# Performance work log

Hardware: AMD Instinct MI355X
Metric: run time of the kernel (lower is better)

## Reference

```python
import jax, jax.numpy as jnp
import numpy as np

N_NODES = 50000
N_EDGES = 1_600_000
HIDDEN = 128
BOND = 16


def setup_inputs() -> dict:
    key = jax.random.key(0)
    ks = jax.random.split(key, 6)
    h = jax.random.normal(ks[0], (N_NODES, HIDDEN), dtype=jnp.float32)
    edge_index = jax.random.randint(ks[1], (2, N_EDGES), 0, N_NODES, dtype=jnp.int32)
    bond_features = jax.random.normal(ks[2], (N_EDGES, BOND), dtype=jnp.float32)
    fan_in1 = 2 * HIDDEN + BOND
    W1 = jax.random.normal(ks[3], (fan_in1, HIDDEN), dtype=jnp.float32) / np.sqrt(fan_in1)
    b1 = jnp.zeros((HIDDEN,), dtype=jnp.float32)
    W2 = jax.random.normal(ks[4], (HIDDEN, HIDDEN), dtype=jnp.float32) / np.sqrt(HIDDEN)
    b2 = jnp.zeros((HIDDEN,), dtype=jnp.float32)
    return {"h": h, "edge_index": edge_index, "bond_features": bond_features,
            "W1": W1, "b1": b1, "W2": W2, "b2": b2}


def reference(h, edge_index, bond_features, W1, b1, W2, b2):
    row, col = edge_index[0], edge_index[1]
    # gather endpoint features + bond features -> [E, 2H+B]
    msgs = jnp.concatenate([h[row], h[col], bond_features], axis=-1)
    # 2-layer MLP with SiLU
    msgs = jax.nn.silu(msgs @ W1 + b1) @ W2 + b2  # [E, H]
    # scatter-add back to source nodes (index_add_ on row)
    h_out = jax.ops.segment_sum(msgs, row, num_segments=h.shape[0])
    return h_out
```

## Files before the change

### kernel.cpp

```cpp
#include <hip/hip_runtime.h>

typedef __attribute__((ext_vector_type(4))) float  f32x4;
typedef __attribute__((ext_vector_type(2))) float  f32x2;
typedef __attribute__((ext_vector_type(8))) short  s16x8;
typedef __attribute__((ext_vector_type(4))) float  f4v;
typedef __attribute__((ext_vector_type(4))) int    i32x4;

#define MFMA_BF16 __builtin_amdgcn_mfma_f32_16x16x32_bf16
#define SENT 0x7fffffff

#if defined(__has_builtin)
#if __has_builtin(__builtin_amdgcn_cvt_pk_fp8_f32) && __has_builtin(__builtin_amdgcn_cvt_pk_f32_fp8)
#define HW8 1
#endif
#endif

__device__ __forceinline__ short f2bf(float f) {
  unsigned u = __builtin_bit_cast(unsigned, f);
  u += 0x7fffu + ((u >> 16) & 1u);
  return (short)(u >> 16);
}
__device__ __forceinline__ float bf2f(short s) {
  unsigned u = ((unsigned)(unsigned short)s) << 16;
  return __builtin_bit_cast(float, u);
}
__device__ __forceinline__ s16x8 cvt8(f4v f0, f4v f1) {
  s16x8 r;
  r[0] = f2bf(f0[0]); r[1] = f2bf(f0[1]); r[2] = f2bf(f0[2]); r[3] = f2bf(f0[3]);
  r[4] = f2bf(f1[0]); r[5] = f2bf(f1[1]); r[6] = f2bf(f1[2]); r[7] = f2bf(f1[3]);
  return r;
}
__device__ __forceinline__ unsigned cvtpk_bf16(float a, float b) {
  unsigned r;
  asm("v_cvt_pk_bf16_f32 %0, %1, %2" : "=v"(r) : "v"(a), "v"(b));
  return r;
}
__device__ __forceinline__ unsigned f2fp8(float x) {
  unsigned u = __builtin_bit_cast(unsigned, x);
  unsigned s = (u >> 24) & 0x80u;
  unsigned au = u & 0x7fffffffu;
  if (au < 0x3C800000u) return s;
  unsigned biased = au - 0x3C000000u;
  unsigned val = biased >> 20;
  unsigned rem = biased & 0xFFFFFu;
  val += (rem > 0x80000u) || (rem == 0x80000u && (val & 1u));
  if (val > 0x7Eu) val = 0x7Eu;
  return s | val;
}
__device__ __forceinline__ float fp8tof(unsigned b) {
  unsigned em = b & 0x7fu;
  unsigned f = ((em + 960u) << 20) | ((b & 0x80u) << 24);
  return (em < 8u) ? 0.f : __builtin_bit_cast(float, f);
}
__device__ __forceinline__ unsigned char enc_fp8(float x) {
#ifdef HW8
  return (unsigned char)(__builtin_amdgcn_cvt_pk_fp8_f32(x, x, 0u, false) & 0xffu);
#else
  return (unsigned char)f2fp8(x);
#endif
}
__device__ __forceinline__ void dec_fp8x4(unsigned d, float* f) {
#ifdef HW8
  f32x2 lo = __builtin_amdgcn_cvt_pk_f32_fp8(d, false);
  f32x2 hi = __builtin_amdgcn_cvt_pk_f32_fp8(d, true);
  f[0] = lo[0]; f[1] = lo[1]; f[2] = hi[0]; f[3] = hi[1];
#else
#pragma unroll
  for (int j = 0; j < 4; ++j) f[j] = fp8tof((d >> (8 * j)) & 0xffu);
#endif
}

__global__ __launch_bounds__(256) void prep_weights(
    const float* __restrict__ W1, const float* __restrict__ W2,
    short* __restrict__ wp) {
  int t = blockIdx.x * 256 + threadIdx.x;
  int chunk = t >> 6, l = t & 63;
  if (chunk >= 104) return;
  int q = l >> 4, c = l & 15;
  s16x8 v;
  if (chunk < 72) {
    int kk = chunk >> 3, nt = chunk & 7;
    int k0 = kk * 32 + q * 8, n = nt * 16 + c;
#pragma unroll
    for (int j = 0; j < 8; ++j) {
      int k = k0 + j;
      v[j] = (k < 272) ? f2bf(W1[k * 128 + n]) : (short)0;
    }
    *reinterpret_cast<s16x8*>(wp + (size_t)chunk * 512 + l * 8) = v;
  } else {
    int c2 = chunk - 72;
    int kk = c2 >> 3, nt = c2 & 7;
    int k0 = kk * 32 + q * 8, n = nt * 16 + c;
#pragma unroll
    for (int j = 0; j < 8; ++j) v[j] = f2bf(W2[(k0 + j) * 128 + n]);
    *reinterpret_cast<s16x8*>(wp + 36864 + (size_t)c2 * 512 + l * 8) = v;
  }
}

#define NB_H 512
__global__ __launch_bounds__(256) void k_gh(
    const float* __restrict__ h, const short* __restrict__ wp,
    short* __restrict__ Gs, const int* __restrict__ ei,
    int* __restrict__ cnt, int NN, int NB_G, int E) {
  if ((int)blockIdx.x >= NB_G) {
    int i = ((int)blockIdx.x - NB_G) * 256 + threadIdx.x;
    for (; i < E; i += NB_H * 256) atomicAdd(&cnt[ei[i]], 1);
    return;
  }
  const int tid = threadIdx.x;
  const int w = tid >> 6, l = tid & 63;
  const int q = l >> 4, c = l & 15;
  const int nb = blockIdx.x * 64 + w * 16;

  f32x4 acc[16];
#pragma unroll
  for (int nt = 0; nt < 16; ++nt) acc[nt] = (f32x4){0.f, 0.f, 0.f, 0.f};

#pragma unroll
  for (int kk = 0; kk < 4; ++kk) {
    int node = nb + c; if (node >= NN) node = NN - 1;
    const float* src = h + (size_t)node * 128 + kk * 32 + q * 8;
    s16x8 a = cvt8(*reinterpret_cast<const f4v*>(src),
                   *reinterpret_cast<const f4v*>(src + 4));
#pragma unroll
    for (int nt2 = 0; nt2 < 16; ++nt2) {
      int kkg = kk + ((nt2 >= 8) ? 4 : 0);
      int chunk = kkg * 8 + (nt2 & 7);
      s16x8 b = *reinterpret_cast<const s16x8*>(wp + (size_t)chunk * 512 + l * 8);
      acc[nt2] = MFMA_BF16(a, b, acc[nt2], 0, 0, 0);
    }
  }
  unsigned char* Gb = (unsigned char*)Gs;
#pragma unroll
  for (int nt2 = 0; nt2 < 16; ++nt2)
#pragma unroll
    for (int r = 0; r < 4; ++r) {
      int node = nb + q * 4 + r;
      if (node < NN) {
        if (nt2 < 8) {
          Gs[(size_t)node * 192 + nt2 * 16 + c] = f2bf(acc[nt2][r]);
        } else {
          int n7 = nt2 - 8;
          int addr = ((n7 & 1) * 2 + (c >> 3)) * 32 + (n7 >> 1) * 8 + (c & 7);
          Gb[(size_t)node * 384 + 256 + addr] = enc_fp8(acc[nt2][r]);
        }
      }
    }
}

__global__ __launch_bounds__(1024) void k_s1(const int* __restrict__ cnt,
                                             int* __restrict__ partial, int NN) {
  __shared__ int red[16];
  int t = threadIdx.x, idx = blockIdx.x * 1024 + t;
  int v = (idx < NN) ? cnt[idx] : 0;
#pragma unroll
  for (int d = 1; d < 64; d <<= 1) v += __shfl_xor(v, d);
  if ((t & 63) == 0) red[t >> 6] = v;
  __syncthreads();
  if (t == 0) {
    int s = 0;
#pragma unroll
    for (int i = 0; i < 16; ++i) s += red[i];
    partial[blockIdx.x] = s;
  }
}
__global__ __launch_bounds__(1024) void k_s2(int* __restrict__ partial, int P) {
  __shared__ int ps[1024];
  int t = threadIdx.x;
  int v = (t < P) ? partial[t] : 0;
  ps[t] = v; __syncthreads();
  for (int d = 1; d < 1024; d <<= 1) {
    int u = (t >= d) ? ps[t - d] : 0;
    __syncthreads(); ps[t] += u; __syncthreads();
  }
  if (t < P) partial[t] = ps[t] - v;
}
__global__ __launch_bounds__(1024) void k_s3(int* __restrict__ cnt,
                                             const int* __restrict__ partial, int NN) {
  __shared__ int ps[1024];
  int t = threadIdx.x, idx = blockIdx.x * 1024 + t;
  int v = (idx < NN) ? cnt[idx] : 0;
  ps[t] = v; __syncthreads();
  for (int d = 1; d < 1024; d <<= 1) {
    int u = (t >= d) ? ps[t - d] : 0;
    __syncthreads(); ps[t] += u; __syncthreads();
  }
  if (idx < NN) cnt[idx] = ps[t] - v + partial[blockIdx.x];
}

__global__ void k_scatter8(const int* __restrict__ ei, int* __restrict__ cnt,
                           int* __restrict__ rc, short* __restrict__ bond_s,
                           const float* __restrict__ bond, int E) {
  int i = blockIdx.x * blockDim.x + threadIdx.x;
  int stride = gridDim.x * blockDim.x;
  for (; i < E; i += stride) {
    int r = ei[i], c = ei[(size_t)E + i];
    int pos = atomicAdd(&cnt[r], 1);
    rc[pos] = r | (c << 16);
    const f4v* b4 = reinterpret_cast<const f4v*>(bond + (size_t)i * 16);
    s16x8 lo = cvt8(b4[0], b4[1]);
    s16x8 hi = cvt8(b4[2], b4[3]);
    s16x8* dst = reinterpret_cast<s16x8*>(bond_s + (size_t)pos * 16);
    dst[0] = lo;
    dst[1] = hi;
  }
}

__global__ void k_scatter(const int* __restrict__ ei, int* __restrict__ cnt,
                          int2* __restrict__ rce, int E) {
  int i = blockIdx.x * blockDim.x + threadIdx.x;
  int stride = gridDim.x * blockDim.x;
  for (; i < E; i += stride) {
    int r = ei[i], c = ei[(size_t)E + i];
    int pos = atomicAdd(&cnt[r], 1);
    rce[pos] = make_int2(r | (c << 16), i);
  }
}

__global__ __launch_bounds__(256, 4) void edge_mlp8(
    const short* __restrict__ Gs, const int* __restrict__ rc,
    const short* __restrict__ bond_s, const short* __restrict__ wp,
    const float* __restrict__ b1, const float* __restrict__ b2,
    float* __restrict__ out, int E) {
  __shared__ __align__(16) char ubuf[4 * 16 * 136 * 2];
  short (*Plds)[16][136] = reinterpret_cast<short(*)[16][136]>(ubuf);
  float (*Sred)[16][68]  = reinterpret_cast<float(*)[16][68]>(ubuf);
  __shared__ int rows_s[64];
  __shared__ int cols_s[64];

  const int tid = threadIdx.x;
  const int w = tid >> 6, l = tid & 63;
  const int q = l >> 4, c = l & 15;

  int nwg = gridDim.x;
  int qq = nwg >> 3, rr = nwg & 7;
  int xcd = blockIdx.x & 7, idx = blockIdx.x >> 3;
  int sbid = (xcd < rr ? xcd * (qq + 1) : rr * (qq + 1) + (xcd - rr) * qq) + idx;
  const int eb = sbid * 64;

  if (tid < 64) {
    int gpos = eb + tid;
    if (gpos < E) {
      int v = rc[gpos];
      rows_s[tid] = v & 0xffff;
      cols_s[tid] = ((unsigned)v) >> 16;
    } else {
      rows_s[tid] = SENT; cols_s[tid] = 0;
    }
  }
  __syncthreads();

  const int we = w * 16;
  int el = we + c;
  int rv = rows_s[el];
  int rA = (rv == SENT) ? 0 : rv;
  int cA = cols_s[el];

  unsigned long long bm = __ballot(
      (l < 16) && (rows_s[we + l] != ((l < 15) ? rows_s[we + l + 1] : -1)));

  s16x8 g1v[4];
  i32x4 g2v[2];
  s16x8 az = {};
  {
    const short* gb = Gs + (size_t)rA * 192;
#pragma unroll
    for (int kk = 0; kk < 4; ++kk)
      g1v[kk] = *reinterpret_cast<const s16x8*>(gb + kk * 32 + q * 8);
    const char* g2b = (const char*)Gs + (size_t)cA * 384 + 256 + q * 32;
    g2v[0] = *reinterpret_cast<const i32x4*>(g2b);
    g2v[1] = *reinterpret_cast<const i32x4*>(g2b + 16);
    if (q < 2) {
      int ge = eb + we + c; if (ge >= E) ge = E - 1;
      az = *reinterpret_cast<const s16x8*>(bond_s + (size_t)ge * 16 + q * 8);
    }
  }

  f32x4 accb[8];
#pragma unroll
  for (int nt = 0; nt < 8; ++nt) accb[nt] = (f32x4){0.f, 0.f, 0.f, 0.f};
#pragma unroll
  for (int nt = 0; nt < 8; ++nt) {
    s16x8 b = *reinterpret_cast<const s16x8*>(wp + (size_t)(64 + nt) * 512 + l * 8);
    accb[nt] = MFMA_BF16(az, b, accb[nt], 0, 0, 0);
  }

#pragma unroll
  for (int nt = 0; nt < 8; ++nt) {
    float bias = b1[nt * 16 + c];
#pragma unroll
    for (int r = 0; r < 4; ++r)
      Plds[w][q * 4 + r][nt * 16 + c] = f2bf(accb[nt][r] + bias);
  }

  f32x4 acc2[8];
#pragma unroll
  for (int nt = 0; nt < 8; ++nt) acc2[nt] = (f32x4){0.f, 0.f, 0.f, 0.f};

#pragma unroll
  for (int kk = 0; kk < 4; ++kk) {
    s16x8 gk = g1v[kk];
    unsigned d0 = (unsigned)g2v[kk >> 1][(kk & 1) * 2 + 0];
    unsigned d1 = (unsigned)g2v[kk >> 1][(kk & 1) * 2 + 1];
    float g2f[8];
    dec_fp8x4(d0, g2f);
    dec_fp8x4(d1, g2f + 4);
    s16x8 pb = *reinterpret_cast<const s16x8*>(&Plds[w][c][kk * 32 + q * 8]);
    float sv[8];
#pragma unroll
    for (int j = 0; j < 8; ++j) {
      float x = bf2f(gk[j]) + g2f[j] + bf2f(pb[j]);
      float e = __expf(-x);
      sv[j] = x * __builtin_amdgcn_rcpf(1.f + e);
    }
    i32x4 a2w;
#pragma unroll
    for (int p = 0; p < 4; ++p)
      a2w[p] = (int)cvtpk_bf16(sv[2 * p], sv[2 * p + 1]);
    s16x8 a2 = __builtin_bit_cast(s16x8, a2w);
#pragma unroll
    for (int nt = 0; nt < 8; ++nt) {
      s16x8 b = *reinterpret_cast<const s16x8*>(wp + 36864 + (size_t)(kk * 8 + nt) * 512 + l * 8);
      acc2[nt] = MFMA_BF16(a2, b, acc2[nt], 0, 0, 0);
    }
  }

#pragma unroll
  for (int h2 = 0; h2 < 2; ++h2) {
    if (h2) __syncthreads();
#pragma unroll
    for (int nt2 = 0; nt2 < 4; ++nt2) {
      int nt = h2 * 4 + nt2;
      float bias = b2[nt * 16 + c];
#pragma unroll
      for (int r = 0; r < 4; ++r)
        Sred[w][q * 4 + r][nt2 * 16 + c] = acc2[nt][r] + bias;
    }
    float vsum = 0.f;
#pragma unroll
    for (int r = 0; r < 16; ++r) {
      vsum += Sred[w][r][l];
      if ((bm >> r) & 1ull) {
        int rowv = rows_s[we + r];
        if (rowv != SENT)
          unsafeAtomicAdd(&out[(size_t)rowv * 128 + h2 * 64 + l], vsum);
        vsum = 0.f;
      }
    }
  }
}

__global__ __launch_bounds__(256, 4) void edge_mlp7(
    const short* __restrict__ Gs, const int2* __restrict__ rce,
    const float* __restrict__ bond, const short* __restrict__ wp,
    const float* __restrict__ b1, const float* __restrict__ b2,
    float* __restrict__ out, int E) {
  __shared__ __align__(16) char ubuf[4 * 16 * 136 * 2];
  short (*Plds)[16][136] = reinterpret_cast<short(*)[16][136]>(ubuf);
  float (*Sred)[16][68]  = reinterpret_cast<float(*)[16][68]>(ubuf);
  __shared__ int rows_s[64];
  __shared__ int cols_s[64];
  __shared__ int eidx_s[64];

  const int tid = threadIdx.x;
  const int w = tid >> 6, l = tid & 63;
  const int q = l >> 4, c = l & 15;

  int nwg = gridDim.x;
  int qq = nwg >> 3, rr = nwg & 7;
  int xcd = blockIdx.x & 7, idx = blockIdx.x >> 3;
  int sbid = (xcd < rr ? xcd * (qq + 1) : rr * (qq + 1) + (xcd - rr) * qq) + idx;
  const int eb = sbid * 64;

  if (tid < 64) {
    int gpos = eb + tid;
    if (gpos < E) {
      int2 v = rce[gpos];
      rows_s[tid] = v.x & 0xffff;
      cols_s[tid] = ((unsigned)v.x) >> 16;
      eidx_s[tid] = v.y;
    } else {
      rows_s[tid] = SENT; cols_s[tid] = 0; eidx_s[tid] = 0;
    }
  }
  __syncthreads();

  const int we = w * 16;
  int el = we + c;
  int rv = rows_s[el];
  int rA = (rv == SENT) ? 0 : rv;
  int cA = cols_s[el];
  int eA = eidx_s[el];

  unsigned long long bm = __ballot(
      (l < 16) && (rows_s[we + l] != ((l < 15) ? rows_s[we + l + 1] : -1)));

  s16x8 g1v[4];
  i32x4 g2v[2];
  {
    const short* gb = Gs + (size_t)rA * 192;
#pragma unroll
    for (int kk = 0; kk < 4; ++kk)
      g1v[kk] = *reinterpret_cast<const s16x8*>(gb + kk * 32 + q * 8);
    const char* g2b = (const char*)Gs + (size_t)cA * 384 + 256 + q * 32;
    g2v[0] = *reinterpret_cast<const i32x4*>(g2b);
    g2v[1] = *reinterpret_cast<const i32x4*>(g2b + 16);
  }

  f32x4 accb[8];
#pragma unroll
  for (int nt = 0; nt < 8; ++nt) accb[nt] = (f32x4){0.f, 0.f, 0.f, 0.f};
  {
    s16x8 a = {};
    if (q < 2) {
      const float* src = bond + (size_t)eA * 16 + q * 8;
      a = cvt8(*reinterpret_cast<const f4v*>(src),
               *reinterpret_cast<const f4v*>(src + 4));
    }
#pragma unroll
    for (int nt = 0; nt < 8; ++nt) {
      s16x8 b = *reinterpret_cast<const s16x8*>(wp + (size_t)(64 + nt) * 512 + l * 8);
      accb[nt] = MFMA_BF16(a, b, accb[nt], 0, 0, 0);
    }
  }

#pragma unroll
  for (int nt = 0; nt < 8; ++nt) {
    float bias = b1[nt * 16 + c];
#pragma unroll
    for (int r = 0; r < 4; ++r)
      Plds[w][q * 4 + r][nt * 16 + c] = f2bf(accb[nt][r] + bias);
  }

  f32x4 acc2[8];
#pragma unroll
  for (int nt = 0; nt < 8; ++nt) acc2[nt] = (f32x4){0.f, 0.f, 0.f, 0.f};

#pragma unroll
  for (int kk = 0; kk < 4; ++kk) {
    s16x8 gk = g1v[kk];
    unsigned d0 = (unsigned)g2v[kk >> 1][(kk & 1) * 2 + 0];
    unsigned d1 = (unsigned)g2v[kk >> 1][(kk & 1) * 2 + 1];
    float g2f[8];
    dec_fp8x4(d0, g2f);
    dec_fp8x4(d1, g2f + 4);
    s16x8 pb = *reinterpret_cast<const s16x8*>(&Plds[w][c][kk * 32 + q * 8]);
    s16x8 a2;
#pragma unroll
    for (int j = 0; j < 8; ++j) {
      float x = bf2f(gk[j]) + g2f[j] + bf2f(pb[j]);
      float e = __expf(-x);
      float s = x * __builtin_amdgcn_rcpf(1.f + e);
      a2[j] = f2bf(s);
    }
#pragma unroll
    for (int nt = 0; nt < 8; ++nt) {
      s16x8 b = *reinterpret_cast<const s16x8*>(wp + 36864 + (size_t)(kk * 8 + nt) * 512 + l * 8);
      acc2[nt] = MFMA_BF16(a2, b, acc2[nt], 0, 0, 0);
    }
  }

#pragma unroll
  for (int h2 = 0; h2 < 2; ++h2) {
    if (h2) __syncthreads();
#pragma unroll
    for (int nt2 = 0; nt2 < 4; ++nt2) {
      int nt = h2 * 4 + nt2;
      float bias = b2[nt * 16 + c];
#pragma unroll
      for (int r = 0; r < 4; ++r)
        Sred[w][q * 4 + r][nt2 * 16 + c] = acc2[nt][r] + bias;
    }
    float vsum = 0.f;
#pragma unroll
    for (int r = 0; r < 16; ++r) {
      vsum += Sred[w][r][l];
      if ((bm >> r) & 1ull) {
        int rowv = rows_s[we + r];
        if (rowv != SENT)
          unsafeAtomicAdd(&out[(size_t)rowv * 128 + h2 * 64 + l], vsum);
        vsum = 0.f;
      }
    }
  }
}

__global__ __launch_bounds__(256, 2) void edge_mlp(
    const float* __restrict__ h, const int* __restrict__ ei,
    const float* __restrict__ bond, const short* __restrict__ wp,
    const float* __restrict__ b1, const float* __restrict__ b2,
    float* __restrict__ out, int E) {
  __shared__ __align__(16) short Plds[4][64][136];
  __shared__ int rows_s[256];
  __shared__ int cols_s[256];
  const int tid = threadIdx.x;
  const int w = tid >> 6, l = tid & 63;
  const int q = l >> 4, c = l & 15;
  const int eb = blockIdx.x * 256;
  {
    int e = eb + tid; if (e >= E) e = E - 1;
    rows_s[tid] = ei[e];
    cols_s[tid] = ei[(size_t)E + e];
  }
  __syncthreads();
  const int we = w * 64;
  int rN[4], cN[4], eI[4];
#pragma unroll
  for (int mi = 0; mi < 4; ++mi) {
    int el = we + mi * 16 + c;
    rN[mi] = rows_s[el]; cN[mi] = cols_s[el];
    int eg = eb + el; if (eg >= E) eg = E - 1;
    eI[mi] = eg;
  }
  f32x4 acc[4][8];
#pragma unroll
  for (int mi = 0; mi < 4; ++mi)
#pragma unroll
    for (int nt = 0; nt < 8; ++nt) acc[mi][nt] = (f32x4){0.f, 0.f, 0.f, 0.f};
#pragma unroll
  for (int part = 0; part < 2; ++part) {
#pragma unroll
    for (int kk = 0; kk < 4; ++kk) {
      s16x8 a[4];
#pragma unroll
      for (int mi = 0; mi < 4; ++mi) {
        int node = part ? cN[mi] : rN[mi];
        const float* src = h + (size_t)node * 128 + kk * 32 + q * 8;
        a[mi] = cvt8(*reinterpret_cast<const f4v*>(src),
                     *reinterpret_cast<const f4v*>(src + 4));
      }
      const int kkg = part * 4 + kk;
#pragma unroll
      for (int nt = 0; nt < 8; ++nt) {
        s16x8 b = *reinterpret_cast<const s16x8*>(wp + (size_t)(kkg * 8 + nt) * 512 + l * 8);
#pragma unroll
        for (int mi = 0; mi < 4; ++mi)
          acc[mi][nt] = MFMA_BF16(a[mi], b, acc[mi][nt], 0, 0, 0);
      }
    }
  }
  {
    s16x8 a[4];
#pragma unroll
    for (int mi = 0; mi < 4; ++mi) {
      s16x8 az = {};
      if (q < 2) {
        const float* src = bond + (size_t)eI[mi] * 16 + q * 8;
        az = cvt8(*reinterpret_cast<const f4v*>(src),
                  *reinterpret_cast<const f4v*>(src + 4));
      }
      a[mi] = az;
    }
#pragma unroll
    for (int nt = 0; nt < 8; ++nt) {
      s16x8 b = *reinterpret_cast<const s16x8*>(wp + (size_t)(64 + nt) * 512 + l * 8);
#pragma unroll
      for (int mi = 0; mi < 4; ++mi)
        acc[mi][nt] = MFMA_BF16(a[mi], b, acc[mi][nt], 0, 0, 0);
    }
  }
#pragma unroll
  for (int nt = 0; nt < 8; ++nt) {
    float bias = b1[nt * 16 + c];
#pragma unroll
    for (int mi = 0; mi < 4; ++mi)
#pragma unroll
      for (int r = 0; r < 4; ++r) {
        float x = acc[mi][nt][r] + bias;
        float s = x / (1.f + __expf(-x));
        Plds[w][mi * 16 + q * 4 + r][nt * 16 + c] = f2bf(s);
      }
  }
  f32x4 acc2[4][8];
#pragma unroll
  for (int mi = 0; mi < 4; ++mi)
#pragma unroll
    for (int nt = 0; nt < 8; ++nt) acc2[mi][nt] = (f32x4){0.f, 0.f, 0.f, 0.f};
#pragma unroll
  for (int kk = 0; kk < 4; ++kk) {
    s16x8 a2[4];
#pragma unroll
    for (int mi = 0; mi < 4; ++mi)
      a2[mi] = *reinterpret_cast<const s16x8*>(&Plds[w][mi * 16 + c][kk * 32 + q * 8]);
#pragma unroll
    for (int nt = 0; nt < 8; ++nt) {
      s16x8 b = *reinterpret_cast<const s16x8*>(wp + 36864 + (size_t)(kk * 8 + nt) * 512 + l * 8);
#pragma unroll
      for (int mi = 0; mi < 4; ++mi)
        acc2[mi][nt] = MFMA_BF16(a2[mi], b, acc2[mi][nt], 0, 0, 0);
    }
  }
#pragma unroll
  for (int nt = 0; nt < 8; ++nt) {
    float bias = b2[nt * 16 + c];
#pragma unroll
    for (int mi = 0; mi < 4; ++mi)
#pragma unroll
      for (int r = 0; r < 4; ++r) {
        int el = we + mi * 16 + q * 4 + r;
        if ((eb + el) < E) {
          int node = rows_s[el];
          unsafeAtomicAdd(&out[(size_t)node * 128 + nt * 16 + c],
                          acc2[mi][nt][r] + bias);
        }
      }
  }
}

extern "C" void kernel_launch(void* const* d_in, const int* in_sizes, int n_in,
                              void* d_out, int out_size, void* d_ws, size_t ws_size,
                              hipStream_t stream) {
  const float* h    = (const float*)d_in[0];
  const int*   ei   = (const int*)d_in[1];
  const float* bond = (const float*)d_in[2];
  const float* W1   = (const float*)d_in[3];
  const float* b1   = (const float*)d_in[4];
  const float* W2   = (const float*)d_in[5];
  const float* b2   = (const float*)d_in[6];
  float* out = (float*)d_out;
  char* ws = (char*)d_ws;

  const int E  = in_sizes[1] / 2;
  const int NN = in_sizes[0] / 128;

  short* wp = (short*)ws;
  size_t off_G    = 131072;
  size_t off_cnt  = off_G + (size_t)NN * 384;
  size_t off_par  = off_cnt + (((size_t)NN * 4 + 15) & ~15ull);
  size_t off_idx  = off_par + 4096;
  size_t off_bs   = off_idx + (((size_t)E * 4 + 15) & ~15ull);
  size_t need8    = off_bs + (size_t)E * 32;
  size_t need7    = off_idx + (size_t)E * 8;

  hipMemsetAsync(d_out, 0, (size_t)NN * 128 * sizeof(float), stream);
  prep_weights<<<26, 256, 0, stream>>>(W1, W2, wp);

  if (ws_size >= need8 && NN <= 65535) {
    short* Gs     = (short*)(ws + off_G);
    int*   cnt    = (int*)(ws + off_cnt);
    int*   par    = (int*)(ws + off_par);
    int*   rc     = (int*)(ws + off_idx);
    short* bond_s = (short*)(ws + off_bs);
    const int NB_G = (NN + 63) / 64;
    const int P    = (NN + 1023) / 1024;

    hipMemsetAsync(cnt, 0, (size_t)NN * 4, stream);
    k_gh<<<NB_G + NB_H, 256, 0, stream>>>(h, wp, Gs, ei, cnt, NN, NB_G, E);
    k_s1<<<P, 1024, 0, stream>>>(cnt, par, NN);
    k_s2<<<1, 1024, 0, stream>>>(par, P);
    k_s3<<<P, 1024, 0, stream>>>(cnt, par, NN);
    k_scatter8<<<2048, 256, 0, stream>>>(ei, cnt, rc, bond_s, bond, E);
    edge_mlp8<<<(E + 63) / 64, 256, 0, stream>>>(Gs, rc, bond_s, wp, b1, b2, out, E);
  } else if (ws_size >= need7 && NN <= 65535) {
    short* Gs   = (short*)(ws + off_G);
    int*   cnt  = (int*)(ws + off_cnt);
    int*   par  = (int*)(ws + off_par);
    int2*  rce  = (int2*)(ws + off_idx);
    const int NB_G = (NN + 63) / 64;
    const int P    = (NN + 1023) / 1024;

    hipMemsetAsync(cnt, 0, (size_t)NN * 4, stream);
    k_gh<<<NB_G + NB_H, 256, 0, stream>>>(h, wp, Gs, ei, cnt, NN, NB_G, E);
    k_s1<<<P, 1024, 0, stream>>>(cnt, par, NN);
    k_s2<<<1, 1024, 0, stream>>>(par, P);
    k_s3<<<P, 1024, 0, stream>>>(cnt, par, NN);
    k_scatter<<<2048, 256, 0, stream>>>(ei, cnt, rce, E);
    edge_mlp7<<<(E + 63) / 64, 256, 0, stream>>>(Gs, rce, bond, wp, b1, b2, out, E);
  } else {
    edge_mlp<<<(E + 255) / 256, 256, 0, stream>>>(h, ei, bond, wp, b1, b2, out, E);
  }
}
```

Before: 440.3 us.

## Process two 64-edge groups per block with all gathers issued upfront

Each block of the edge MLP kernel now handles 128 sorted edges instead of 64. The node-feature, fp8 column-feature and bond gathers for both groups are issued before any compute, so the second group's memory latency is hidden behind the first group's MFMA work, and weight reloads are spread over twice as many edges. The cost is higher register pressure from holding two sets of gathered operands, which could cause spills or lower occupancy under the 256x4 launch bounds, and the grid has half as many blocks.

```diff
diff --git a/kernel.cpp b/kernel.cpp
--- a/kernel.cpp
+++ b/kernel.cpp
@@ -217,7 +217,7 @@
   }
 }
 
-__global__ __launch_bounds__(256, 4) void edge_mlp8(
+__global__ __launch_bounds__(256, 4) void edge_mlp9(
     const short* __restrict__ Gs, const int* __restrict__ rc,
     const short* __restrict__ bond_s, const short* __restrict__ wp,
     const float* __restrict__ b1, const float* __restrict__ b2,
@@ -225,8 +225,8 @@
   __shared__ __align__(16) char ubuf[4 * 16 * 136 * 2];
   short (*Plds)[16][136] = reinterpret_cast<short(*)[16][136]>(ubuf);
   float (*Sred)[16][68]  = reinterpret_cast<float(*)[16][68]>(ubuf);
-  __shared__ int rows_s[64];
-  __shared__ int cols_s[64];
+  __shared__ int rows_s[128];
+  __shared__ int cols_s[128];
 
   const int tid = threadIdx.x;
   const int w = tid >> 6, l = tid & 63;
@@ -236,9 +236,9 @@
   int qq = nwg >> 3, rr = nwg & 7;
   int xcd = blockIdx.x & 7, idx = blockIdx.x >> 3;
   int sbid = (xcd < rr ? xcd * (qq + 1) : rr * (qq + 1) + (xcd - rr) * qq) + idx;
-  const int eb = sbid * 64;
-
-  if (tid < 64) {
+  const int eb = sbid * 128;
+
+  if (tid < 128) {
     int gpos = eb + tid;
     if (gpos < E) {
       int v = rc[gpos];
@@ -251,100 +251,113 @@
   __syncthreads();
 
   const int we = w * 16;
-  int el = we + c;
-  int rv = rows_s[el];
-  int rA = (rv == SENT) ? 0 : rv;
-  int cA = cols_s[el];
-
-  unsigned long long bm = __ballot(
-      (l < 16) && (rows_s[we + l] != ((l < 15) ? rows_s[we + l + 1] : -1)));
-
-  s16x8 g1v[4];
-  i32x4 g2v[2];
-  s16x8 az = {};
-  {
-    const short* gb = Gs + (size_t)rA * 192;
+  int rA[2], cA[2];
+  unsigned long long bm[2];
+#pragma unroll
+  for (int g = 0; g < 2; ++g) {
+    int el = g * 64 + we + c;
+    int rv = rows_s[el];
+    rA[g] = (rv == SENT) ? 0 : rv;
+    cA[g] = cols_s[el];
+    bm[g] = __ballot(
+        (l < 16) &&
+        (rows_s[g * 64 + we + l] != ((l < 15) ? rows_s[g * 64 + we + l + 1] : -1)));
+  }
+
+  s16x8 g1v[2][4];
+  i32x4 g2v[2][2];
+  s16x8 az[2];
+#pragma unroll
+  for (int g = 0; g < 2; ++g) {
+    const short* gb = Gs + (size_t)rA[g] * 192;
 #pragma unroll
     for (int kk = 0; kk < 4; ++kk)
-      g1v[kk] = *reinterpret_cast<const s16x8*>(gb + kk * 32 + q * 8);
-    const char* g2b = (const char*)Gs + (size_t)cA * 384 + 256 + q * 32;
-    g2v[0] = *reinterpret_cast<const i32x4*>(g2b);
-    g2v[1] = *reinterpret_cast<const i32x4*>(g2b + 16);
+      g1v[g][kk] = *reinterpret_cast<const s16x8*>(gb + kk * 32 + q * 8);
+    const char* g2b = (const char*)Gs + (size_t)cA[g] * 384 + 256 + q * 32;
+    g2v[g][0] = *reinterpret_cast<const i32x4*>(g2b);
+    g2v[g][1] = *reinterpret_cast<const i32x4*>(g2b + 16);
+    s16x8 a0 = {};
     if (q < 2) {
-      int ge = eb + we + c; if (ge >= E) ge = E - 1;
-      az = *reinterpret_cast<const s16x8*>(bond_s + (size_t)ge * 16 + q * 8);
-    }
-  }
-
-  f32x4 accb[8];
-#pragma unroll
-  for (int nt = 0; nt < 8; ++nt) accb[nt] = (f32x4){0.f, 0.f, 0.f, 0.f};
-#pragma unroll
-  for (int nt = 0; nt < 8; ++nt) {
-    s16x8 b = *reinterpret_cast<const s16x8*>(wp + (size_t)(64 + nt) * 512 + l * 8);
-    accb[nt] = MFMA_BF16(az, b, accb[nt], 0, 0, 0);
-  }
-
-#pragma unroll
-  for (int nt = 0; nt < 8; ++nt) {
-    float bias = b1[nt * 16 + c];
-#pragma unroll
-    for (int r = 0; r < 4; ++r)
-      Plds[w][q * 4 + r][nt * 16 + c] = f2bf(accb[nt][r] + bias);
-  }
-
-  f32x4 acc2[8];
-#pragma unroll
-  for (int nt = 0; nt < 8; ++nt) acc2[nt] = (f32x4){0.f, 0.f, 0.f, 0.f};
-
-#pragma unroll
-  for (int kk = 0; kk < 4; ++kk) {
-    s16x8 gk = g1v[kk];
-    unsigned d0 = (unsigned)g2v[kk >> 1][(kk & 1) * 2 + 0];
-    unsigned d1 = (unsigned)g2v[kk >> 1][(kk & 1) * 2 + 1];
-    float g2f[8];
-    dec_fp8x4(d0, g2f);
-    dec_fp8x4(d1, g2f + 4);
-    s16x8 pb = *reinterpret_cast<const s16x8*>(&Plds[w][c][kk * 32 + q * 8]);
-    float sv[8];
-#pragma unroll
-    for (int j = 0; j < 8; ++j) {
-      float x = bf2f(gk[j]) + g2f[j] + bf2f(pb[j]);
-      float e = __expf(-x);
-      sv[j] = x * __builtin_amdgcn_rcpf(1.f + e);
-    }
-    i32x4 a2w;
-#pragma unroll
-    for (int p = 0; p < 4; ++p)
-      a2w[p] = (int)cvtpk_bf16(sv[2 * p], sv[2 * p + 1]);
-    s16x8 a2 = __builtin_bit_cast(s16x8, a2w);
+      int ge = eb + g * 64 + we + c; if (ge >= E) ge = E - 1;
+      a0 = *reinterpret_cast<const s16x8*>(bond_s + (size_t)ge * 16 + q * 8);
+    }
+    az[g] = a0;
+  }
+
+#pragma unroll
+  for (int g = 0; g < 2; ++g) {
+    if (g) __syncthreads();
+
+    f32x4 accb[8];
+#pragma unroll
+    for (int nt = 0; nt < 8; ++nt) accb[nt] = (f32x4){0.f, 0.f, 0.f, 0.f};
 #pragma unroll
     for (int nt = 0; nt < 8; ++nt) {
-      s16x8 b = *reinterpret_cast<const s16x8*>(wp + 36864 + (size_t)(kk * 8 + nt) * 512 + l * 8);
-      acc2[nt] = MFMA_BF16(a2, b, acc2[nt], 0, 0, 0);
-    }
-  }
-
-#pragma unroll
-  for (int h2 = 0; h2 < 2; ++h2) {
-    if (h2) __syncthreads();
-#pragma unroll
-    for (int nt2 = 0; nt2 < 4; ++nt2) {
-      int nt = h2 * 4 + nt2;
-      float bias = b2[nt * 16 + c];
+      s16x8 b = *reinterpret_cast<const s16x8*>(wp + (size_t)(64 + nt) * 512 + l * 8);
+      accb[nt] = MFMA_BF16(az[g], b, accb[nt], 0, 0, 0);
+    }
+
+#pragma unroll
+    for (int nt = 0; nt < 8; ++nt) {
+      float bias = b1[nt * 16 + c];
 #pragma unroll
       for (int r = 0; r < 4; ++r)
-        Sred[w][q * 4 + r][nt2 * 16 + c] = acc2[nt][r] + bias;
-    }
-    float vsum = 0.f;
-#pragma unroll
-    for (int r = 0; r < 16; ++r) {
-      vsum += Sred[w][r][l];
-      if ((bm >> r) & 1ull) {
-        int rowv = rows_s[we + r];
-        if (rowv != SENT)
-          unsafeAtomicAdd(&out[(size_t)rowv * 128 + h2 * 64 + l], vsum);
-        vsum = 0.f;
+        Plds[w][q * 4 + r][nt * 16 + c] = f2bf(accb[nt][r] + bias);
+    }
+
+    f32x4 acc2[8];
+#pragma unroll
+    for (int nt = 0; nt < 8; ++nt) acc2[nt] = (f32x4){0.f, 0.f, 0.f, 0.f};
+
+#pragma unroll
+    for (int kk = 0; kk < 4; ++kk) {
+      s16x8 gk = g1v[g][kk];
+      unsigned d0 = (unsigned)g2v[g][kk >> 1][(kk & 1) * 2 + 0];
+      unsigned d1 = (unsigned)g2v[g][kk >> 1][(kk & 1) * 2 + 1];
+      float g2f[8];
+      dec_fp8x4(d0, g2f);
+      dec_fp8x4(d1, g2f + 4);
+      s16x8 pb = *reinterpret_cast<const s16x8*>(&Plds[w][c][kk * 32 + q * 8]);
+      float sv[8];
+#pragma unroll
+      for (int j = 0; j < 8; ++j) {
+        float x = bf2f(gk[j]) + g2f[j] + bf2f(pb[j]);
+        float e = __expf(-x);
+        sv[j] = x * __builtin_amdgcn_rcpf(1.f + e);
+      }
+      i32x4 a2w;
+#pragma unroll
+      for (int p = 0; p < 4; ++p)
+        a2w[p] = (int)cvtpk_bf16(sv[2 * p], sv[2 * p + 1]);
+      s16x8 a2 = __builtin_bit_cast(s16x8, a2w);
+#pragma unroll
+      for (int nt = 0; nt < 8; ++nt) {
+        s16x8 b = *reinterpret_cast<const s16x8*>(wp + 36864 + (size_t)(kk * 8 + nt) * 512 + l * 8);
+        acc2[nt] = MFMA_BF16(a2, b, acc2[nt], 0, 0, 0);
+      }
+    }
+
+#pragma unroll
+    for (int h2 = 0; h2 < 2; ++h2) {
+      if (h2) __syncthreads();
+#pragma unroll
+      for (int nt2 = 0; nt2 < 4; ++nt2) {
+        int nt = h2 * 4 + nt2;
+        float bias = b2[nt * 16 + c];
+#pragma unroll
+        for (int r = 0; r < 4; ++r)
+          Sred[w][q * 4 + r][nt2 * 16 + c] = acc2[nt][r] + bias;
+      }
+      float vsum = 0.f;
+#pragma unroll
+      for (int r = 0; r < 16; ++r) {
+        vsum += Sred[w][r][l];
+        if ((bm[g] >> r) & 1ull) {
+          int rowv = rows_s[g * 64 + we + r];
+          if (rowv != SENT)
+            unsafeAtomicAdd(&out[(size_t)rowv * 128 + h2 * 64 + l], vsum);
+          vsum = 0.f;
+        }
       }
     }
   }
@@ -629,13 +642,13 @@
   size_t off_par  = off_cnt + (((size_t)NN * 4 + 15) & ~15ull);
   size_t off_idx  = off_par + 4096;
   size_t off_bs   = off_idx + (((size_t)E * 4 + 15) & ~15ull);
-  size_t need8    = off_bs + (size_t)E * 32;
+  size_t need9    = off_bs + (size_t)E * 32;
   size_t need7    = off_idx + (size_t)E * 8;
 
   hipMemsetAsync(d_out, 0, (size_t)NN * 128 * sizeof(float), stream);
   prep_weights<<<26, 256, 0, stream>>>(W1, W2, wp);
 
-  if (ws_size >= need8 && NN <= 65535) {
+  if (ws_size >= need9 && NN <= 65535) {
     short* Gs     = (short*)(ws + off_G);
     int*   cnt    = (int*)(ws + off_cnt);
     int*   par    = (int*)(ws + off_par);
@@ -650,7 +663,7 @@
     k_s2<<<1, 1024, 0, stream>>>(par, P);
     k_s3<<<P, 1024, 0, stream>>>(cnt, par, NN);
     k_scatter8<<<2048, 256, 0, stream>>>(ei, cnt, rc, bond_s, bond, E);
-    edge_mlp8<<<(E + 63) / 64, 256, 0, stream>>>(Gs, rc, bond_s, wp, b1, b2, out, E);
+    edge_mlp9<<<(E + 127) / 128, 256, 0, stream>>>(Gs, rc, bond_s, wp, b1, b2, out, E);
   } else if (ws_size >= need7 && NN <= 65535) {
     short* Gs   = (short*)(ws + off_G);
     int*   cnt  = (int*)(ws + off_cnt);
```

Result: slower. 464.6 us (+5.5%).
